# Kernel optimization log

Measured on AMD Instinct MI355X. Metric: run time of the kernel, lower is better.

The kernel has to match this reference:

```python
import jax, jax.numpy as jnp
import numpy as np

H = 16  # num heads
HD = 64  # head dim


def setup_inputs() -> dict:
    key = jax.random.key(0)
    ks = jax.random.split(key, 7)
    B, T, C = 4, 2048, 1024
    s = 0.02
    return {
        "x": jax.random.normal(ks[0], (B, T, C), jnp.float32),
        "pos_emb": jax.random.normal(ks[1], (1, T, C), jnp.float32),
        "w_attn": jax.random.normal(ks[2], (C, 3 * C), jnp.float32) * s,
        "b_attn": jax.random.normal(ks[3], (3 * C,), jnp.float32) * s,
        "w_proj": jax.random.normal(ks[4], (C, C), jnp.float32) * s,
        "b_proj": jax.random.normal(ks[5], (C,), jnp.float32) * s,
    }


def reference(x, pos_emb, w_attn, b_attn, w_proj, b_proj):
    B, T, C = x.shape
    qkv = x @ w_attn + b_attn  # [B,T,3C]
    q, k, v = jnp.split(qkv, 3, axis=2)
    # special positional embedding added to q and k (pre head-split)
    q = q + pos_emb
    k = k + pos_emb

    def split_heads(t):
        return t.reshape(B, T, H, HD).transpose(0, 2, 1, 3)  # [B,H,T,HD]

    q, k, v = split_heads(q), split_heads(k), split_heads(v)
    att = jnp.einsum("bhqd,bhkd->bhqk", q, k) / jnp.sqrt(jnp.float32(HD))
    causal = jnp.tril(jnp.ones((T, T), bool))
    att = jnp.where(causal[None, None], att, -jnp.inf)
    att = jax.nn.softmax(att, axis=-1)
    y = jnp.einsum("bhqk,bhkd->bhqd", att, v)
    y = y.transpose(0, 2, 1, 3).reshape(B, T, C)
    y = y @ w_proj + b_proj
    return (y, k, v)
```

## Files before the change

### kernel.cpp

```cpp
#include <hip/hip_runtime.h>
#include <hip/hip_bf16.h>
#include <stdint.h>

#define B_  4
#define T_  2048
#define C_  1024
#define H_  16
#define HD_ 64
#define YSZ 8388608

typedef __attribute__((ext_vector_type(8))) __bf16 bf16x8;
typedef __attribute__((ext_vector_type(4))) float  f32x4;

__device__ __forceinline__ ushort f2bf(float x) {
  union { float f; uint32_t u; } v; v.f = x;
  uint32_t r = v.u + 0x7FFFu + ((v.u >> 16) & 1u);
  return (ushort)(r >> 16);
}

__device__ __forceinline__ void async16(void* lds, const void* g) {
  __builtin_amdgcn_global_load_lds(
      (const __attribute__((address_space(1))) void*)g,
      (__attribute__((address_space(3))) void*)lds, 16, 0, 0);
}

__global__ __launch_bounds__(256) void k_cvt(const float* __restrict__ in,
                                             ushort* __restrict__ out, int n4) {
  int i = blockIdx.x * 256 + threadIdx.x;
  if (i < n4) {
    const float4 v = ((const float4*)in)[i];
    ushort4 o; o.x = f2bf(v.x); o.y = f2bf(v.y); o.z = f2bf(v.z); o.w = f2bf(v.w);
    ((ushort4*)out)[i] = o;
  }
}

__global__ __launch_bounds__(256) void k_transpose_bf16(const float* __restrict__ in,
                                                        ushort* __restrict__ out,
                                                        int rows, int cols) {
  __shared__ float tile[32][33];
  const int bx = blockIdx.x * 32;
  const int by = blockIdx.y * 32;
  const int tx = threadIdx.x & 31;
  const int ty = threadIdx.x >> 5;
#pragma unroll
  for (int j = 0; j < 4; ++j)
    tile[ty + j * 8][tx] = in[(size_t)(by + ty + j * 8) * cols + bx + tx];
  __syncthreads();
#pragma unroll
  for (int j = 0; j < 4; ++j)
    out[(size_t)(bx + ty + j * 8) * rows + by + tx] = f2bf(tile[tx][ty + j * 8]);
}

template <int MODE>
__global__ __launch_bounds__(256) void k_gemm(
    const ushort* __restrict__ A, const ushort* __restrict__ Bt,
    const float* __restrict__ bias, const float* __restrict__ pos,
    float* __restrict__ outY, ushort* __restrict__ qbf, ushort* __restrict__ kbf,
    ushort* __restrict__ vtbf, int M, int N, int K) {
  __shared__ ushort Ab[128 * 64];
  __shared__ ushort Bb[128 * 64];
  const int tid = threadIdx.x;
  const int wid = tid >> 6, lane = tid & 63;
  const int wr = wid >> 1, wc = wid & 1;
  const int g = lane >> 4, c = lane & 15;
  const int bm = blockIdx.x * 128;
  const int bn = blockIdx.y * 128;

  f32x4 acc[4][4] = {};

  const int r0 = wid * 8 + (lane >> 3);
  const int ch = lane & 7;

  for (int kt = 0; kt < K; kt += 64) {
    __syncthreads();
#pragma unroll
    for (int rnd = 0; rnd < 4; ++rnd) {
      const int r = rnd * 32 + r0;
      const int gc = (ch ^ (r & 7)) << 3;
      async16((char*)Ab + rnd * 4096 + wid * 1024,
              A + (size_t)(bm + r) * K + kt + gc);
      async16((char*)Bb + rnd * 4096 + wid * 1024,
              Bt + (size_t)(bn + r) * K + kt + gc);
    }
    __syncthreads();
#pragma unroll
    for (int ks = 0; ks < 2; ++ks) {
      bf16x8 af[4], bfr[4];
#pragma unroll
      for (int m = 0; m < 4; ++m) {
        const int row = wr * 64 + m * 16 + c;
        const int bir = (ks * 64 + g * 16) ^ ((row & 7) << 4);
        af[m] = *(const bf16x8*)((const char*)Ab + row * 128 + bir);
      }
#pragma unroll
      for (int n = 0; n < 4; ++n) {
        const int row = wc * 64 + n * 16 + c;
        const int bir = (ks * 64 + g * 16) ^ ((row & 7) << 4);
        bfr[n] = *(const bf16x8*)((const char*)Bb + row * 128 + bir);
      }
#pragma unroll
      for (int m = 0; m < 4; ++m)
#pragma unroll
        for (int n = 0; n < 4; ++n)
          acc[m][n] = __builtin_amdgcn_mfma_f32_16x16x32_bf16(af[m], bfr[n],
                                                              acc[m][n], 0, 0, 0);
    }
  }

  const float QSC = 0.125f * 1.4426950408889634f;
#pragma unroll
  for (int m = 0; m < 4; ++m) {
    const int rowbase = bm + wr * 64 + m * 16 + g * 4;
#pragma unroll
    for (int n = 0; n < 4; ++n) {
      const int col = bn + wc * 64 + n * 16 + c;
#pragma unroll
      for (int j = 0; j < 4; ++j) {
        const int i = rowbase + j;
        float val = acc[m][n][j] + bias[col];
        if (MODE == 1) {
          outY[(size_t)i * N + col] = val;
        } else {
          const int b = i >> 11, t = i & 2047;
          if (col < C_) {
            val += pos[t * C_ + col];
            const int h = col >> 6, hd = col & 63;
            const size_t o = (((size_t)(b * H_ + h)) * T_ + t) * HD_ + hd;
            qbf[o] = f2bf(val * QSC);
          } else if (col < 2 * C_) {
            const int cc = col - C_;
            val += pos[t * C_ + cc];
            const int h = cc >> 6, hd = cc & 63;
            const size_t o = (((size_t)(b * H_ + h)) * T_ + t) * HD_ + hd;
            outY[(size_t)YSZ + o] = val;
            kbf[o] = f2bf(val);
          } else {
            const int cc = col - 2 * C_;
            const int h = cc >> 6, hd = cc & 63;
            const size_t o = (((size_t)(b * H_ + h)) * T_ + t) * HD_ + hd;
            outY[(size_t)(2 * YSZ) + o] = val;
            vtbf[(((size_t)(b * H_ + h)) * HD_ + hd) * T_ + t] = f2bf(val);
          }
        }
      }
    }
  }
}

__global__ __launch_bounds__(256) void k_attn(const ushort* __restrict__ qbf,
                                              const ushort* __restrict__ kbf,
                                              const ushort* __restrict__ vtbf,
                                              ushort* __restrict__ yatt) {
  __shared__ ushort Kb[2][64 * 64];
  __shared__ ushort Vb[2][64 * 64];
  __shared__ ushort Pb[4][2048];
  const int tid = threadIdx.x;
  const int wid = tid >> 6, lane = tid & 63;
  const int g = lane >> 4, c = lane & 15;
  const int bh = blockIdx.y;
  const size_t bhT = (size_t)bh * T_ * 64;
  const int r0 = wid * 8 + (lane >> 3);
  const int ch = lane & 7;
  const int b = bh >> 4, h = bh & 15;

  auto stage = [&](int buf, int t) {
    const int kv0 = t * 64;
#pragma unroll
    for (int rnd = 0; rnd < 2; ++rnd) {
      const int r = rnd * 32 + r0;
      const int gc = (ch ^ (r & 7)) << 3;
      async16((char*)Kb[buf] + rnd * 4096 + wid * 1024,
              kbf + bhT + (size_t)(kv0 + r) * 64 + gc);
      async16((char*)Vb[buf] + rnd * 4096 + wid * 1024,
              vtbf + bhT + (size_t)r * T_ + kv0 + gc);
    }
  };

  for (int half = 0; half < 2; ++half) {
    const int qtile = half ? (15 - (int)blockIdx.x) : (int)blockIdx.x;
    const int qbase = qtile * 128;
    const int ntiles = qtile * 2 + 2;
    const int qmin = qbase + wid * 32;

    bf16x8 qf[2][2];
#pragma unroll
    for (int m = 0; m < 2; ++m)
#pragma unroll
      for (int ks = 0; ks < 2; ++ks)
        qf[m][ks] = *(const bf16x8*)(qbf + bhT +
                                     (size_t)(qbase + wid * 32 + m * 16 + c) * 64 +
                                     ks * 32 + g * 8);

    f32x4 o[2][4] = {};
    float mrow[2][4], lrow[2][4];
#pragma unroll
    for (int m = 0; m < 2; ++m)
#pragma unroll
      for (int j = 0; j < 4; ++j) { mrow[m][j] = -__builtin_inff(); lrow[m][j] = 0.f; }

    for (int t = 0; t < ntiles; ++t) {
      if (t == 0) {
        __syncthreads();
        stage(0, 0);
      }
      __syncthreads();
      if (t + 1 < ntiles) stage((t + 1) & 1, t + 1);

      const char* kb = (const char*)Kb[t & 1];
      const char* vb = (const char*)Vb[t & 1];
      const int kv0 = t * 64;

      f32x4 s[2][4] = {};
      __builtin_amdgcn_s_setprio(1);
#pragma unroll
      for (int ks = 0; ks < 2; ++ks) {
        bf16x8 kf[4];
#pragma unroll
        for (int n = 0; n < 4; ++n) {
          const int row = n * 16 + c;
          const int bir = (ks * 64 + g * 16) ^ ((row & 7) << 4);
          kf[n] = *(const bf16x8*)(kb + row * 128 + bir);
        }
#pragma unroll
        for (int m = 0; m < 2; ++m)
#pragma unroll
          for (int n = 0; n < 4; ++n)
            s[m][n] = __builtin_amdgcn_mfma_f32_16x16x32_bf16(qf[m][ks], kf[n],
                                                              s[m][n], 0, 0, 0);
      }
      __builtin_amdgcn_s_setprio(0);

      const bool needmask = (kv0 + 63 > qmin);
      if (needmask) {
#pragma unroll
        for (int m = 0; m < 2; ++m)
#pragma unroll
          for (int n = 0; n < 4; ++n) {
            const int kvi = kv0 + n * 16 + c;
#pragma unroll
            for (int j = 0; j < 4; ++j) {
              const int qi = qbase + wid * 32 + m * 16 + g * 4 + j;
              if (kvi > qi) s[m][n][j] = -__builtin_inff();
            }
          }
      }

#pragma unroll
      for (int m = 0; m < 2; ++m)
#pragma unroll
        for (int j = 0; j < 4; ++j) {
          float mx = fmaxf(fmaxf(s[m][0][j], s[m][1][j]),
                           fmaxf(s[m][2][j], s[m][3][j]));
#pragma unroll
          for (int w = 1; w < 16; w <<= 1) mx = fmaxf(mx, __shfl_xor(mx, w));
          const float mnew = fmaxf(mrow[m][j], mx);
          const float corr = exp2f(mrow[m][j] - mnew);
          float rs = 0.f;
#pragma unroll
          for (int n = 0; n < 4; ++n) {
            const float pv = exp2f(s[m][n][j] - mnew);
            s[m][n][j] = pv;
            rs += pv;
          }
#pragma unroll
          for (int w = 1; w < 16; w <<= 1) rs += __shfl_xor(rs, w);
          lrow[m][j] = lrow[m][j] * corr + rs;
          mrow[m][j] = mnew;
#pragma unroll
          for (int n = 0; n < 4; ++n) o[m][n][j] *= corr;
        }

      asm volatile("" ::: "memory");
      char* pb = (char*)&Pb[wid][0];
#pragma unroll
      for (int m = 0; m < 2; ++m)
#pragma unroll
        for (int n = 0; n < 4; ++n)
#pragma unroll
          for (int j = 0; j < 4; ++j) {
            const int row = m * 16 + g * 4 + j;
            const int byte = row * 128 + ((((n * 16 + c) * 2)) ^ ((row & 7) << 4));
            *(ushort*)(pb + byte) = f2bf(s[m][n][j]);
          }
      asm volatile("" ::: "memory");

      __builtin_amdgcn_s_setprio(1);
#pragma unroll
      for (int ks = 0; ks < 2; ++ks) {
        bf16x8 pf[2], vf[4];
#pragma unroll
        for (int m = 0; m < 2; ++m) {
          const int row = m * 16 + c;
          const int bir = (ks * 64 + g * 16) ^ ((row & 7) << 4);
          pf[m] = *(const bf16x8*)(pb + row * 128 + bir);
        }
#pragma unroll
        for (int n = 0; n < 4; ++n) {
          const int row = n * 16 + c;
          const int bir = (ks * 64 + g * 16) ^ ((row & 7) << 4);
          vf[n] = *(const bf16x8*)(vb + row * 128 + bir);
        }
#pragma unroll
        for (int m = 0; m < 2; ++m)
#pragma unroll
          for (int n = 0; n < 4; ++n)
            o[m][n] = __builtin_amdgcn_mfma_f32_16x16x32_bf16(pf[m], vf[n],
                                                              o[m][n], 0, 0, 0);
      }
      __builtin_amdgcn_s_setprio(0);
    }

#pragma unroll
    for (int m = 0; m < 2; ++m)
#pragma unroll
      for (int j = 0; j < 4; ++j) {
        const float inv = 1.0f / lrow[m][j];
        const int qi = qbase + wid * 32 + m * 16 + g * 4 + j;
        const size_t rowoff = ((size_t)b * T_ + qi) * C_ + h * 64;
#pragma unroll
        for (int n = 0; n < 4; ++n)
          yatt[rowoff + n * 16 + c] = f2bf(o[m][n][j] * inv);
      }
  }
}

extern "C" void kernel_launch(void* const* d_in, const int* in_sizes, int n_in,
                              void* d_out, int out_size, void* d_ws, size_t ws_size,
                              hipStream_t stream) {
  (void)in_sizes; (void)n_in; (void)out_size;
  const float* x      = (const float*)d_in[0];
  const float* pos    = (const float*)d_in[1];
  const float* w_attn = (const float*)d_in[2];
  const float* b_attn = (const float*)d_in[3];
  const float* w_proj = (const float*)d_in[4];
  const float* b_proj = (const float*)d_in[5];
  float* out = (float*)d_out;

  if (ws_size < (size_t)(88u << 20)) return;
  char* ws = (char*)d_ws;
  ushort* xbf  = (ushort*)(ws);
  ushort* waT  = (ushort*)(ws + (16 << 20));
  ushort* wpT  = (ushort*)(ws + (22 << 20));
  ushort* qbf  = (ushort*)(ws + (24 << 20));
  ushort* kbf  = (ushort*)(ws + (40 << 20));
  ushort* vtbf = (ushort*)(ws + (56 << 20));
  ushort* yatt = (ushort*)(ws + (72 << 20));

  k_cvt<<<8192, 256, 0, stream>>>(x, xbf, 2097152);
  k_transpose_bf16<<<dim3(96, 32), 256, 0, stream>>>(w_attn, waT, 1024, 3072);
  k_transpose_bf16<<<dim3(32, 32), 256, 0, stream>>>(w_proj, wpT, 1024, 1024);
  k_gemm<0><<<dim3(64, 24), 256, 0, stream>>>(xbf, waT, b_attn, pos, out, qbf, kbf,
                                              vtbf, 8192, 3072, 1024);
  k_attn<<<dim3(8, 64), 256, 0, stream>>>(qbf, kbf, vtbf, yatt);
  k_gemm<1><<<dim3(64, 8), 256, 0, stream>>>(yatt, wpT, b_proj, nullptr, out, nullptr,
                                             nullptr, nullptr, 8192, 1024, 1024);
}
```

Measured before the change: 429.8 us.

## Transpose attention MFMAs so each lane owns a query row; lazy rescale softmax

Swaps the operand order of the QK^T and PV MFMAs so the accumulator is transposed and each lane holds all scores for a single query column. Row max and sum then need only two cross-lane shuffles instead of four per row. The change also adds a lazy-rescale rule that keeps the old max when the new max exceeds it by at most 8 (in log2 units) across the whole wave, skipping the correction exp and output rescale. P is packed to bf16 with v_cvt_pk_bf16_f32 and written as 8-byte stores. The lazy threshold trades some headroom in fp32/bf16 range for fewer rescales, and the output store pattern changes to four consecutive elements per lane.

```diff
diff --git a/kernel.cpp b/kernel.cpp
--- a/kernel.cpp
+++ b/kernel.cpp
@@ -16,6 +16,12 @@
   union { float f; uint32_t u; } v; v.f = x;
   uint32_t r = v.u + 0x7FFFu + ((v.u >> 16) & 1u);
   return (ushort)(r >> 16);
+}
+
+__device__ __forceinline__ uint32_t cvt_pk_bf16(float lo, float hi) {
+  uint32_t r;
+  asm("v_cvt_pk_bf16_f32 %0, %1, %2" : "=v"(r) : "v"(lo), "v"(hi));
+  return r;
 }
 
 __device__ __forceinline__ void async16(void* lds, const void* g) {
@@ -181,6 +187,7 @@
     const int qbase = qtile * 128;
     const int ntiles = qtile * 2 + 2;
     const int qmin = qbase + wid * 32;
+    const int qcol0 = qbase + wid * 32 + c;
 
     bf16x8 qf[2][2];
 #pragma unroll
@@ -191,12 +198,10 @@
                                      (size_t)(qbase + wid * 32 + m * 16 + c) * 64 +
                                      ks * 32 + g * 8);
 
-    f32x4 o[2][4] = {};
-    float mrow[2][4], lrow[2][4];
-#pragma unroll
-    for (int m = 0; m < 2; ++m)
-#pragma unroll
-      for (int j = 0; j < 4; ++j) { mrow[m][j] = -__builtin_inff(); lrow[m][j] = 0.f; }
+    f32x4 o2[4][2] = {};
+    float mrow[2], lrow[2];
+#pragma unroll
+    for (int m = 0; m < 2; ++m) { mrow[m] = -__builtin_inff(); lrow[m] = 0.f; }
 
     for (int t = 0; t < ntiles; ++t) {
       if (t == 0) {
@@ -210,7 +215,7 @@
       const char* vb = (const char*)Vb[t & 1];
       const int kv0 = t * 64;
 
-      f32x4 s[2][4] = {};
+      f32x4 s2[4][2] = {};
       __builtin_amdgcn_s_setprio(1);
 #pragma unroll
       for (int ks = 0; ks < 2; ++ks) {
@@ -222,66 +227,75 @@
           kf[n] = *(const bf16x8*)(kb + row * 128 + bir);
         }
 #pragma unroll
-        for (int m = 0; m < 2; ++m)
-#pragma unroll
-          for (int n = 0; n < 4; ++n)
-            s[m][n] = __builtin_amdgcn_mfma_f32_16x16x32_bf16(qf[m][ks], kf[n],
-                                                              s[m][n], 0, 0, 0);
+        for (int n = 0; n < 4; ++n)
+#pragma unroll
+          for (int m = 0; m < 2; ++m)
+            s2[n][m] = __builtin_amdgcn_mfma_f32_16x16x32_bf16(kf[n], qf[m][ks],
+                                                               s2[n][m], 0, 0, 0);
       }
       __builtin_amdgcn_s_setprio(0);
 
-      const bool needmask = (kv0 + 63 > qmin);
-      if (needmask) {
-#pragma unroll
-        for (int m = 0; m < 2; ++m)
-#pragma unroll
-          for (int n = 0; n < 4; ++n) {
-            const int kvi = kv0 + n * 16 + c;
-#pragma unroll
-            for (int j = 0; j < 4; ++j) {
-              const int qi = qbase + wid * 32 + m * 16 + g * 4 + j;
-              if (kvi > qi) s[m][n][j] = -__builtin_inff();
-            }
+      if (kv0 + 63 > qmin) {
+#pragma unroll
+        for (int n = 0; n < 4; ++n)
+#pragma unroll
+          for (int j = 0; j < 4; ++j) {
+            const int kvi = kv0 + n * 16 + 4 * g + j;
+#pragma unroll
+            for (int m = 0; m < 2; ++m)
+              if (kvi > qcol0 + m * 16) s2[n][m][j] = -__builtin_inff();
           }
       }
 
 #pragma unroll
-      for (int m = 0; m < 2; ++m)
-#pragma unroll
-        for (int j = 0; j < 4; ++j) {
-          float mx = fmaxf(fmaxf(s[m][0][j], s[m][1][j]),
-                           fmaxf(s[m][2][j], s[m][3][j]));
-#pragma unroll
-          for (int w = 1; w < 16; w <<= 1) mx = fmaxf(mx, __shfl_xor(mx, w));
-          const float mnew = fmaxf(mrow[m][j], mx);
-          const float corr = exp2f(mrow[m][j] - mnew);
-          float rs = 0.f;
-#pragma unroll
-          for (int n = 0; n < 4; ++n) {
-            const float pv = exp2f(s[m][n][j] - mnew);
-            s[m][n][j] = pv;
+      for (int m = 0; m < 2; ++m) {
+        float pmax = s2[0][m][0];
+#pragma unroll
+        for (int n = 0; n < 4; ++n)
+#pragma unroll
+          for (int j = 0; j < 4; ++j) pmax = fmaxf(pmax, s2[n][m][j]);
+        pmax = fmaxf(pmax, __shfl_xor(pmax, 16));
+        pmax = fmaxf(pmax, __shfl_xor(pmax, 32));
+        const bool skip = __all(pmax - mrow[m] <= 8.0f);
+        const float mnew = skip ? mrow[m] : pmax;
+        float rs = 0.f;
+#pragma unroll
+        for (int n = 0; n < 4; ++n)
+#pragma unroll
+          for (int j = 0; j < 4; ++j) {
+            const float pv = exp2f(s2[n][m][j] - mnew);
+            s2[n][m][j] = pv;
             rs += pv;
           }
-#pragma unroll
-          for (int w = 1; w < 16; w <<= 1) rs += __shfl_xor(rs, w);
-          lrow[m][j] = lrow[m][j] * corr + rs;
-          mrow[m][j] = mnew;
-#pragma unroll
-          for (int n = 0; n < 4; ++n) o[m][n][j] *= corr;
-        }
+        rs += __shfl_xor(rs, 16);
+        rs += __shfl_xor(rs, 32);
+        if (skip) {
+          lrow[m] += rs;
+        } else {
+          const float corr = exp2f(mrow[m] - pmax);
+          lrow[m] = lrow[m] * corr + rs;
+          mrow[m] = pmax;
+#pragma unroll
+          for (int n2 = 0; n2 < 4; ++n2)
+#pragma unroll
+            for (int j = 0; j < 4; ++j) o2[n2][m][j] *= corr;
+        }
+      }
 
       asm volatile("" ::: "memory");
       char* pb = (char*)&Pb[wid][0];
 #pragma unroll
-      for (int m = 0; m < 2; ++m)
-#pragma unroll
-        for (int n = 0; n < 4; ++n)
-#pragma unroll
-          for (int j = 0; j < 4; ++j) {
-            const int row = m * 16 + g * 4 + j;
-            const int byte = row * 128 + ((((n * 16 + c) * 2)) ^ ((row & 7) << 4));
-            *(ushort*)(pb + byte) = f2bf(s[m][n][j]);
-          }
+      for (int m = 0; m < 2; ++m) {
+        const int q = m * 16 + c;
+#pragma unroll
+        for (int n = 0; n < 4; ++n) {
+          const uint32_t w0 = cvt_pk_bf16(s2[n][m][0], s2[n][m][1]);
+          const uint32_t w1 = cvt_pk_bf16(s2[n][m][2], s2[n][m][3]);
+          const int kvl = n * 16 + 4 * g;
+          const int byte = q * 128 + ((kvl * 2) ^ ((q & 7) << 4));
+          *(uint2*)(pb + byte) = make_uint2(w0, w1);
+        }
+      }
       asm volatile("" ::: "memory");
 
       __builtin_amdgcn_s_setprio(1);
@@ -301,26 +315,26 @@
           vf[n] = *(const bf16x8*)(vb + row * 128 + bir);
         }
 #pragma unroll
-        for (int m = 0; m < 2; ++m)
-#pragma unroll
-          for (int n = 0; n < 4; ++n)
-            o[m][n] = __builtin_amdgcn_mfma_f32_16x16x32_bf16(pf[m], vf[n],
-                                                              o[m][n], 0, 0, 0);
+        for (int n = 0; n < 4; ++n)
+#pragma unroll
+          for (int m = 0; m < 2; ++m)
+            o2[n][m] = __builtin_amdgcn_mfma_f32_16x16x32_bf16(vf[n], pf[m],
+                                                               o2[n][m], 0, 0, 0);
       }
       __builtin_amdgcn_s_setprio(0);
     }
 
 #pragma unroll
-    for (int m = 0; m < 2; ++m)
-#pragma unroll
-      for (int j = 0; j < 4; ++j) {
-        const float inv = 1.0f / lrow[m][j];
-        const int qi = qbase + wid * 32 + m * 16 + g * 4 + j;
-        const size_t rowoff = ((size_t)b * T_ + qi) * C_ + h * 64;
-#pragma unroll
-        for (int n = 0; n < 4; ++n)
-          yatt[rowoff + n * 16 + c] = f2bf(o[m][n][j] * inv);
-      }
+    for (int m = 0; m < 2; ++m) {
+      const float inv = 1.0f / lrow[m];
+      const int qi = qbase + wid * 32 + m * 16 + c;
+      const size_t rowoff = ((size_t)b * T_ + qi) * C_ + h * 64;
+#pragma unroll
+      for (int n = 0; n < 4; ++n)
+#pragma unroll
+        for (int j = 0; j < 4; ++j)
+          yatt[rowoff + n * 16 + 4 * g + j] = f2bf(o2[n][m][j] * inv);
+    }
   }
 }
 
```

New measurement: 385.1 us. 1.12x faster.
